# Kernel tuning notes

Hardware: AMD Instinct MI355X
Metric: run time of the kernel (lower is better)

Reference implementation:

```python
import jax, jax.numpy as jnp
import numpy as np

HEAD_SIZE = 64
N_EMBD = 1024

def setup_inputs() -> dict:
    key = jax.random.key(0)
    ks = jax.random.split(key, 7)
    B, T = 4, 4096
    s = 1.0 / np.sqrt(N_EMBD)
    return {
        "x": jax.random.normal(ks[0], (B, T, N_EMBD), dtype=jnp.float32),
        "Wq": jax.random.normal(ks[1], (N_EMBD, HEAD_SIZE), dtype=jnp.float32) * s,
        "bq": jnp.zeros((HEAD_SIZE,), dtype=jnp.float32),
        "Wk": jax.random.normal(ks[2], (N_EMBD, HEAD_SIZE), dtype=jnp.float32) * s,
        "bk": jnp.zeros((HEAD_SIZE,), dtype=jnp.float32),
        "Wv": jax.random.normal(ks[3], (N_EMBD, HEAD_SIZE), dtype=jnp.float32) * s,
        "bv": jnp.zeros((HEAD_SIZE,), dtype=jnp.float32),
    }

def reference(x, Wq, bq, Wk, bk, Wv, bv):
    # q,k,v: [B,T,H]
    q = x @ Wq + bq
    k = x @ Wk + bk
    v = x @ Wv + bv
    scale = jnp.asarray(HEAD_SIZE, x.dtype) ** -0.5
    att = jnp.einsum("bth,bsh->bts", q, k) * scale  # [B,T,T]
    att = jax.nn.softmax(att, axis=-1)
    # dropout with p=0.0 is identity (eval-mode reference)
    return jnp.einsum("bts,bsh->bth", att, v)
```

## Files before the change

### kernel.cpp

```cpp
#include <hip/hip_runtime.h>
#include <hip/hip_bf16.h>
#include <cmath>

#define BATCH 4
#define TLEN  4096
#define CEMB  1024
#define HEAD  64
#define NROWS (BATCH * TLEN)

typedef __bf16 bf16;
typedef __attribute__((ext_vector_type(8))) __bf16 bf16x8;
typedef __attribute__((ext_vector_type(4))) __bf16 bf16x4;
typedef __attribute__((ext_vector_type(4))) float f32x4;

#define QSCALE 0.1803368801111204f

static __device__ __forceinline__ f32x4 mfma16(bf16x8 a, bf16x8 b, f32x4 c) {
    return __builtin_amdgcn_mfma_f32_16x16x32_bf16(a, b, c, 0, 0, 0);
}

static __device__ __forceinline__ void async_ld16(const void* g, void* l) {
    __builtin_amdgcn_global_load_lds(
        (const __attribute__((address_space(1))) void*)g,
        (__attribute__((address_space(3))) void*)l, 16, 0, 0);
}

__global__ __launch_bounds__(256) void pack_w(
    const float* __restrict__ Wq, const float* __restrict__ Wk,
    const float* __restrict__ Wv, bf16* __restrict__ Wt)
{
    const int n = blockIdx.x;
    const int which = n >> 6, h = n & 63;
    const float* W = which == 0 ? Wq : (which == 1 ? Wk : Wv);
    const float s = which == 0 ? QSCALE : 1.0f;
    for (int k = threadIdx.x; k < CEMB; k += 256)
        Wt[(size_t)n * CEMB + k] = (bf16)(W[(size_t)k * HEAD + h] * s);
}

__global__ __launch_bounds__(256, 2) void qkv(
    const float* __restrict__ x, const bf16* __restrict__ Wt,
    const float* __restrict__ bq, const float* __restrict__ bk,
    const float* __restrict__ bv,
    bf16* __restrict__ qb, bf16* __restrict__ kb, bf16* __restrict__ vT)
{
    __shared__ __align__(16) float Xsh[2][32][64];

    const int tid  = threadIdx.x;
    const int lane = tid & 63;
    const int wvid = tid >> 6;
    const int quad = lane >> 4;
    const int col  = lane & 15;
    const int row0 = blockIdx.x * 32;

    const float* xblk = x + (size_t)row0 * CEMB;
    const bf16* wrow[3];
    #pragma unroll
    for (int j = 0; j < 3; ++j)
        wrow[j] = Wt + (size_t)((wvid * 3 + j) * 16 + col) * CEMB + quad * 8;

    const int sr = lane >> 4;
    const int ss = lane & 15;
    auto stage = [&](int ci, int bufi) {
        #pragma unroll
        for (int j = 0; j < 2; ++j) {
            const int r = wvid * 8 + j * 4 + sr;
            const int c = ss ^ (r & 7);
            async_ld16(xblk + (size_t)r * CEMB + ci * 64 + c * 4,
                       &Xsh[bufi][wvid * 8 + j * 4][0]);
        }
    };

    f32x4 acc[2][3] = {};
    const int c7 = col & 7;

    stage(0, 0);
    int buf = 0;
    for (int ci = 0; ci < 16; ++ci) {
        __syncthreads();
        if (ci + 1 < 16) stage(ci + 1, buf ^ 1);

        #pragma unroll
        for (int kk = 0; kk < 2; ++kk) {
            const int h = ci * 2 + kk;
            bf16x8 Bv[3];
            #pragma unroll
            for (int j = 0; j < 3; ++j)
                Bv[j] = *(const bf16x8*)(wrow[j] + h * 32);
            #pragma unroll
            for (int rt = 0; rt < 2; ++rt) {
                const int r = rt * 16 + col;
                const int g0 = kk * 8 + quad * 2;
                float4 a0 = *(const float4*)&Xsh[buf][r][(g0 ^ c7) * 4];
                float4 a1 = *(const float4*)&Xsh[buf][r][((g0 + 1) ^ c7) * 4];
                bf16x8 af;
                af[0]=(bf16)a0.x; af[1]=(bf16)a0.y; af[2]=(bf16)a0.z; af[3]=(bf16)a0.w;
                af[4]=(bf16)a1.x; af[5]=(bf16)a1.y; af[6]=(bf16)a1.z; af[7]=(bf16)a1.w;
                #pragma unroll
                for (int j = 0; j < 3; ++j)
                    acc[rt][j] = mfma16(af, Bv[j], acc[rt][j]);
            }
        }
        buf ^= 1;
    }

    const float* bias[3] = {bq, bk, bv};
    #pragma unroll
    for (int j = 0; j < 3; ++j) {
        const int jg = wvid * 3 + j;
        const int which = jg >> 2;
        const int h = (jg & 3) * 16 + col;
        float bb = bias[which][h];
        if (which == 0) bb *= QSCALE;
        #pragma unroll
        for (int rt = 0; rt < 2; ++rt) {
            if (which < 2) {
                bf16* dst = which == 0 ? qb : kb;
                #pragma unroll
                for (int r = 0; r < 4; ++r) {
                    const int trow = row0 + rt * 16 + quad * 4 + r;
                    dst[(size_t)trow * HEAD + h] = (bf16)(acc[rt][j][r] + bb);
                }
            } else {
                bf16x4 pv;
                #pragma unroll
                for (int r = 0; r < 4; ++r) pv[r] = (bf16)(acc[rt][j][r] + bb);
                const int trow0 = row0 + rt * 16 + quad * 4;
                const int bb_   = trow0 >> 12;
                const int tt    = trow0 & (TLEN - 1);
                *(bf16x4*)(vT + ((size_t)(bb_ * HEAD + h)) * TLEN + tt) = pv;
            }
        }
    }
}

__global__ __launch_bounds__(256) void attn(
    const bf16* __restrict__ qb, const bf16* __restrict__ kb,
    const bf16* __restrict__ vT,
    bf16* __restrict__ opart, float* __restrict__ lpart,
    float* __restrict__ out, int nsplit, int lg2S)
{
    __shared__ __align__(16) bf16 Ksh[2][64][64];
    __shared__ __align__(16) bf16 Vsh[2][64][64];
    __shared__ __align__(16) bf16 Psh[4][16][64];

    const int tid  = threadIdx.x;
    const int lane = tid & 63;
    const int wvid = tid >> 6;
    const int quad = lane >> 4;
    const int col  = lane & 15;

    int b, sp, qtile;
    {
        const int id = blockIdx.x;
        if (nsplit >= 2) {
            const int cpx = (BATCH << lg2S) >> 3;
            const int idx = id >> 3;
            const int combo = (id & 7) * cpx + (idx >> 5);
            qtile = idx & 31;
            b = combo >> lg2S;
            sp = combo & (nsplit - 1);
        } else {
            qtile = id & 31; b = id >> 5; sp = 0;
        }
    }
    const int q0 = qtile * 128 + wvid * 32;
    const size_t rowbase = (size_t)b * TLEN + q0;

    bf16x8 qf[2][2];
    #pragma unroll
    for (int qt = 0; qt < 2; ++qt) {
        const bf16* qp = qb + (rowbase + qt * 16 + col) * HEAD + quad * 8;
        qf[qt][0] = *(const bf16x8*)qp;
        qf[qt][1] = *(const bf16x8*)(qp + 32);
    }
    const bf16* kbB = kb + (size_t)b * TLEN * HEAD;
    const bf16* vTB = vT + (size_t)b * HEAD * TLEN;

    f32x4 o[2][4] = {};
    float lsum[2] = {0.f, 0.f};

    const int slen = TLEN >> lg2S;
    const int sbeg = sp * slen;
    const int nch  = slen / 64;

    const int r8 = lane >> 3;
    const int s8 = lane & 7;
    auto stage = [&](int s0, int bufi) {
        #pragma unroll
        for (int j = 0; j < 2; ++j) {
            const int r = wvid * 16 + j * 8 + r8;
            const int c = s8 ^ (r & 7);
            async_ld16(kbB + (size_t)(s0 + r) * HEAD + c * 8,
                       &Ksh[bufi][wvid * 16 + j * 8][0]);
            async_ld16(vTB + (size_t)r * TLEN + s0 + c * 8,
                       &Vsh[bufi][wvid * 16 + j * 8][0]);
        }
    };

    stage(sbeg, 0);
    int buf = 0;
    for (int ci = 0; ci < nch; ++ci) {
        __syncthreads();
        if (ci + 1 < nch) stage(sbeg + (ci + 1) * 64, buf ^ 1);

        const int c7 = col & 7;
        bf16x8 pb[2][2];
        bf16* Pb = &Psh[wvid][col][0];
        #pragma unroll
        for (int qt = 0; qt < 2; ++qt) {
            f32x4 st[4];
            #pragma unroll
            for (int t = 0; t < 4; ++t) {
                const int r = t * 16 + col;
                bf16x8 k0 = *(const bf16x8*)&Ksh[buf][r][(quad ^ c7) * 8];
                bf16x8 k1 = *(const bf16x8*)&Ksh[buf][r][((4 + quad) ^ c7) * 8];
                f32x4 z = {0.f, 0.f, 0.f, 0.f};
                z = mfma16(k0, qf[qt][0], z);
                z = mfma16(k1, qf[qt][1], z);
                st[t] = z;
            }
            #pragma unroll
            for (int t = 0; t < 4; ++t) {
                float p0 = __builtin_amdgcn_exp2f(st[t][0]);
                float p1 = __builtin_amdgcn_exp2f(st[t][1]);
                float p2 = __builtin_amdgcn_exp2f(st[t][2]);
                float p3 = __builtin_amdgcn_exp2f(st[t][3]);
                lsum[qt] += (p0 + p1) + (p2 + p3);
                bf16x4 pv = {(bf16)p0, (bf16)p1, (bf16)p2, (bf16)p3};
                const int g = ((2 * t + (quad >> 1)) ^ c7) * 8 + (quad & 1) * 4;
                *(bf16x4*)(Pb + g) = pv;
            }
            pb[qt][0] = *(const bf16x8*)(Pb + ((quad ^ c7) * 8));
            pb[qt][1] = *(const bf16x8*)(Pb + (((4 + quad) ^ c7) * 8));
        }
        #pragma unroll
        for (int ht = 0; ht < 4; ++ht) {
            const int r = ht * 16 + col;
            bf16x8 v0 = *(const bf16x8*)&Vsh[buf][r][(quad ^ c7) * 8];
            bf16x8 v1 = *(const bf16x8*)&Vsh[buf][r][((4 + quad) ^ c7) * 8];
            o[0][ht] = mfma16(v0, pb[0][0], o[0][ht]);
            o[0][ht] = mfma16(v1, pb[0][1], o[0][ht]);
            o[1][ht] = mfma16(v0, pb[1][0], o[1][ht]);
            o[1][ht] = mfma16(v1, pb[1][1], o[1][ht]);
        }
        buf ^= 1;
    }

    #pragma unroll
    for (int qt = 0; qt < 2; ++qt) {
        lsum[qt] += __shfl_xor(lsum[qt], 16, 64);
        lsum[qt] += __shfl_xor(lsum[qt], 32, 64);
    }

    #pragma unroll
    for (int qt = 0; qt < 2; ++qt) {
        const size_t grow = rowbase + qt * 16 + col;
        if (nsplit == 1) {
            const float inv = 1.f / lsum[qt];
            float* ob = out + grow * HEAD;
            #pragma unroll
            for (int ht = 0; ht < 4; ++ht) {
                f32x4 r = o[qt][ht] * inv;
                *(f32x4*)(ob + ht * 16 + quad * 4) = r;
            }
        } else if (sp == 0) {
            float* ob = out + grow * HEAD;
            #pragma unroll
            for (int ht = 0; ht < 4; ++ht)
                *(f32x4*)(ob + ht * 16 + quad * 4) = o[qt][ht];
            if (quad == 0) lpart[grow] = lsum[qt];
        } else {
            bf16* ob = opart + ((size_t)(sp - 1) * NROWS + grow) * HEAD;
            #pragma unroll
            for (int ht = 0; ht < 4; ++ht) {
                bf16x4 r;
                #pragma unroll
                for (int rr = 0; rr < 4; ++rr) r[rr] = (bf16)o[qt][ht][rr];
                *(bf16x4*)(ob + ht * 16 + quad * 4) = r;
            }
            if (quad == 0) lpart[(size_t)sp * NROWS + grow] = lsum[qt];
        }
    }
}

__global__ __launch_bounds__(256) void combine(
    const bf16* __restrict__ opart, const float* __restrict__ lpart,
    float* __restrict__ out, int nsplit)
{
    const int gid = blockIdx.x * 256 + threadIdx.x;
    const int row = gid >> 4;
    const int h4  = (gid & 15) * 4;

    float L = 0.f;
    for (int s = 0; s < nsplit; ++s) L += lpart[(size_t)s * NROWS + row];
    f32x4 O = *(const f32x4*)(out + (size_t)row * HEAD + h4);
    for (int s = 1; s < nsplit; ++s) {
        bf16x4 v = *(const bf16x4*)(opart + ((size_t)(s - 1) * NROWS + row) * HEAD + h4);
        O[0] += (float)v[0]; O[1] += (float)v[1];
        O[2] += (float)v[2]; O[3] += (float)v[3];
    }
    f32x4 r = O * (1.f / L);
    *(f32x4*)(out + (size_t)row * HEAD + h4) = r;
}

extern "C" void kernel_launch(void* const* d_in, const int* in_sizes, int n_in,
                              void* d_out, int out_size, void* d_ws, size_t ws_size,
                              hipStream_t stream) {
    const float* x  = (const float*)d_in[0];
    const float* Wq = (const float*)d_in[1];
    const float* bq = (const float*)d_in[2];
    const float* Wk = (const float*)d_in[3];
    const float* bk = (const float*)d_in[4];
    const float* Wv = (const float*)d_in[5];
    const float* bv = (const float*)d_in[6];
    float* out = (float*)d_out;

    const size_t n_tok = (size_t)NROWS * HEAD;
    char* ws = (char*)d_ws;
    bf16* qb = (bf16*)ws;
    bf16* kb = qb + n_tok;
    bf16* vT = kb + n_tok;
    bf16* Wt = vT + n_tok;
    const size_t base = 3 * n_tok * sizeof(bf16) + 192 * CEMB * sizeof(bf16);

    auto need = [&](int S) {
        return base + (size_t)(S - 1) * n_tok * sizeof(bf16)
                    + (size_t)S * NROWS * sizeof(float);
    };
    int S = 1, lg2S = 0;
    if      (ws_size >= need(8)) { S = 8; lg2S = 3; }
    else if (ws_size >= need(4)) { S = 4; lg2S = 2; }
    else if (ws_size >= need(2)) { S = 2; lg2S = 1; }
    bf16*  opart = Wt + 192 * CEMB;
    float* lpart = (float*)(opart + (size_t)(S - 1) * n_tok);

    pack_w<<<dim3(192), dim3(256), 0, stream>>>(Wq, Wk, Wv, Wt);
    qkv<<<dim3(512), dim3(256), 0, stream>>>(x, Wt, bq, bk, bv, qb, kb, vT);
    attn<<<dim3(32 * BATCH * S), dim3(256), 0, stream>>>(
        qb, kb, vT, opart, lpart, out, S, lg2S);
    if (S > 1)
        combine<<<dim3((NROWS * 16) / 256), dim3(256), 0, stream>>>(
            opart, lpart, out, S);
}
```

Before: 162.5 us.

## Double query rows per attention wave and deepen QKV projection staging chunks

The attention kernel now has each wave handle 64 query rows instead of 32 and loads K fragments from shared memory once per chunk, reusing them across four query tiles. This halves the grid and the K/V staging traffic per query row. The change also raises register pressure, and launch bounds now request two blocks per CU. Separately, the QKV projection stages 128 input columns per pipeline step instead of 64, halving the number of barriers at the cost of twice the shared memory.

```diff
diff --git a/kernel.cpp b/kernel.cpp
--- a/kernel.cpp
+++ b/kernel.cpp
@@ -43,7 +43,7 @@
     const float* __restrict__ bv,
     bf16* __restrict__ qb, bf16* __restrict__ kb, bf16* __restrict__ vT)
 {
-    __shared__ __align__(16) float Xsh[2][32][64];
+    __shared__ __align__(16) float Xsh[2][2][32][64];
 
     const int tid  = threadIdx.x;
     const int lane = tid & 63;
@@ -62,12 +62,14 @@
     const int ss = lane & 15;
     auto stage = [&](int ci, int bufi) {
         #pragma unroll
-        for (int j = 0; j < 2; ++j) {
-            const int r = wvid * 8 + j * 4 + sr;
-            const int c = ss ^ (r & 7);
-            async_ld16(xblk + (size_t)r * CEMB + ci * 64 + c * 4,
-                       &Xsh[bufi][wvid * 8 + j * 4][0]);
-        }
+        for (int h2 = 0; h2 < 2; ++h2)
+            #pragma unroll
+            for (int j = 0; j < 2; ++j) {
+                const int r = wvid * 8 + j * 4 + sr;
+                const int c = ss ^ (r & 7);
+                async_ld16(xblk + (size_t)r * CEMB + ci * 128 + h2 * 64 + c * 4,
+                           &Xsh[bufi][h2][wvid * 8 + j * 4][0]);
+            }
     };
 
     f32x4 acc[2][3] = {};
@@ -75,13 +77,15 @@
 
     stage(0, 0);
     int buf = 0;
-    for (int ci = 0; ci < 16; ++ci) {
+    for (int ci = 0; ci < 8; ++ci) {
         __syncthreads();
-        if (ci + 1 < 16) stage(ci + 1, buf ^ 1);
-
-        #pragma unroll
-        for (int kk = 0; kk < 2; ++kk) {
-            const int h = ci * 2 + kk;
+        if (ci + 1 < 8) stage(ci + 1, buf ^ 1);
+
+        #pragma unroll
+        for (int kk = 0; kk < 4; ++kk) {
+            const int h  = ci * 4 + kk;
+            const int hf = kk >> 1;
+            const int kl = kk & 1;
             bf16x8 Bv[3];
             #pragma unroll
             for (int j = 0; j < 3; ++j)
@@ -89,9 +93,9 @@
             #pragma unroll
             for (int rt = 0; rt < 2; ++rt) {
                 const int r = rt * 16 + col;
-                const int g0 = kk * 8 + quad * 2;
-                float4 a0 = *(const float4*)&Xsh[buf][r][(g0 ^ c7) * 4];
-                float4 a1 = *(const float4*)&Xsh[buf][r][((g0 + 1) ^ c7) * 4];
+                const int g0 = kl * 8 + quad * 2;
+                float4 a0 = *(const float4*)&Xsh[buf][hf][r][(g0 ^ c7) * 4];
+                float4 a1 = *(const float4*)&Xsh[buf][hf][r][((g0 + 1) ^ c7) * 4];
                 bf16x8 af;
                 af[0]=(bf16)a0.x; af[1]=(bf16)a0.y; af[2]=(bf16)a0.z; af[3]=(bf16)a0.w;
                 af[4]=(bf16)a1.x; af[5]=(bf16)a1.y; af[6]=(bf16)a1.z; af[7]=(bf16)a1.w;
@@ -133,7 +137,7 @@
     }
 }
 
-__global__ __launch_bounds__(256) void attn(
+__global__ __launch_bounds__(256, 2) void attn(
     const bf16* __restrict__ qb, const bf16* __restrict__ kb,
     const bf16* __restrict__ vT,
     bf16* __restrict__ opart, float* __restrict__ lpart,
@@ -155,20 +159,20 @@
         if (nsplit >= 2) {
             const int cpx = (BATCH << lg2S) >> 3;
             const int idx = id >> 3;
-            const int combo = (id & 7) * cpx + (idx >> 5);
-            qtile = idx & 31;
+            const int combo = (id & 7) * cpx + (idx >> 4);
+            qtile = idx & 15;
             b = combo >> lg2S;
             sp = combo & (nsplit - 1);
         } else {
-            qtile = id & 31; b = id >> 5; sp = 0;
-        }
-    }
-    const int q0 = qtile * 128 + wvid * 32;
+            qtile = id & 15; b = id >> 4; sp = 0;
+        }
+    }
+    const int q0 = qtile * 256 + wvid * 64;
     const size_t rowbase = (size_t)b * TLEN + q0;
 
-    bf16x8 qf[2][2];
-    #pragma unroll
-    for (int qt = 0; qt < 2; ++qt) {
+    bf16x8 qf[4][2];
+    #pragma unroll
+    for (int qt = 0; qt < 4; ++qt) {
         const bf16* qp = qb + (rowbase + qt * 16 + col) * HEAD + quad * 8;
         qf[qt][0] = *(const bf16x8*)qp;
         qf[qt][1] = *(const bf16x8*)(qp + 32);
@@ -176,8 +180,8 @@
     const bf16* kbB = kb + (size_t)b * TLEN * HEAD;
     const bf16* vTB = vT + (size_t)b * HEAD * TLEN;
 
-    f32x4 o[2][4] = {};
-    float lsum[2] = {0.f, 0.f};
+    f32x4 o[4][4] = {};
+    float lsum[4] = {0.f, 0.f, 0.f, 0.f};
 
     const int slen = TLEN >> lg2S;
     const int sbeg = sp * slen;
@@ -204,19 +208,23 @@
         if (ci + 1 < nch) stage(sbeg + (ci + 1) * 64, buf ^ 1);
 
         const int c7 = col & 7;
-        bf16x8 pb[2][2];
+        bf16x8 kf[4][2];
+        #pragma unroll
+        for (int t = 0; t < 4; ++t) {
+            const int r = t * 16 + col;
+            kf[t][0] = *(const bf16x8*)&Ksh[buf][r][(quad ^ c7) * 8];
+            kf[t][1] = *(const bf16x8*)&Ksh[buf][r][((4 + quad) ^ c7) * 8];
+        }
+        bf16x8 pb[4][2];
         bf16* Pb = &Psh[wvid][col][0];
         #pragma unroll
-        for (int qt = 0; qt < 2; ++qt) {
+        for (int qt = 0; qt < 4; ++qt) {
             f32x4 st[4];
             #pragma unroll
             for (int t = 0; t < 4; ++t) {
-                const int r = t * 16 + col;
-                bf16x8 k0 = *(const bf16x8*)&Ksh[buf][r][(quad ^ c7) * 8];
-                bf16x8 k1 = *(const bf16x8*)&Ksh[buf][r][((4 + quad) ^ c7) * 8];
                 f32x4 z = {0.f, 0.f, 0.f, 0.f};
-                z = mfma16(k0, qf[qt][0], z);
-                z = mfma16(k1, qf[qt][1], z);
+                z = mfma16(kf[t][0], qf[qt][0], z);
+                z = mfma16(kf[t][1], qf[qt][1], z);
                 st[t] = z;
             }
             #pragma unroll
@@ -238,22 +246,23 @@
             const int r = ht * 16 + col;
             bf16x8 v0 = *(const bf16x8*)&Vsh[buf][r][(quad ^ c7) * 8];
             bf16x8 v1 = *(const bf16x8*)&Vsh[buf][r][((4 + quad) ^ c7) * 8];
-            o[0][ht] = mfma16(v0, pb[0][0], o[0][ht]);
-            o[0][ht] = mfma16(v1, pb[0][1], o[0][ht]);
-            o[1][ht] = mfma16(v0, pb[1][0], o[1][ht]);
-            o[1][ht] = mfma16(v1, pb[1][1], o[1][ht]);
+            #pragma unroll
+            for (int qt = 0; qt < 4; ++qt) {
+                o[qt][ht] = mfma16(v0, pb[qt][0], o[qt][ht]);
+                o[qt][ht] = mfma16(v1, pb[qt][1], o[qt][ht]);
+            }
         }
         buf ^= 1;
     }
 
     #pragma unroll
-    for (int qt = 0; qt < 2; ++qt) {
+    for (int qt = 0; qt < 4; ++qt) {
         lsum[qt] += __shfl_xor(lsum[qt], 16, 64);
         lsum[qt] += __shfl_xor(lsum[qt], 32, 64);
     }
 
     #pragma unroll
-    for (int qt = 0; qt < 2; ++qt) {
+    for (int qt = 0; qt < 4; ++qt) {
         const size_t grow = rowbase + qt * 16 + col;
         if (nsplit == 1) {
             const float inv = 1.f / lsum[qt];
@@ -336,7 +345,7 @@
 
     pack_w<<<dim3(192), dim3(256), 0, stream>>>(Wq, Wk, Wv, Wt);
     qkv<<<dim3(512), dim3(256), 0, stream>>>(x, Wt, bq, bk, bv, qb, kb, vT);
-    attn<<<dim3(32 * BATCH * S), dim3(256), 0, stream>>>(
+    attn<<<dim3(16 * BATCH * S), dim3(256), 0, stream>>>(
         qb, kb, vT, opart, lpart, out, S, lg2S);
     if (S > 1)
         combine<<<dim3((NROWS * 16) / 256), dim3(256), 0, stream>>>(
```

Measured after the change: 161.3 us. About the same (-0.7%).
